# Kernel tuning notes

Measured on AMD Instinct MI355X. Metric: run time of the kernel, lower is better.

The kernel has to match this reference:

```python
import jax, jax.numpy as jnp
import numpy as np

T, B, X, H, Z = 28, 16384, 28, 100, 16
EPS = 1e-10


def setup_inputs() -> dict:
    key = jax.random.key(0)
    ks = jax.random.split(key, 32)
    s = 0.1  # weight scale to keep activations sane
    d = {
        'x': jax.random.uniform(ks[0], (T, B, X), jnp.float32),
        'eps': jax.random.normal(ks[1], (T, B, Z), jnp.float32),
        'Wpx': jax.random.normal(ks[2], (H, X)) * s, 'bpx': jnp.zeros((H,)),
        'Wpz': jax.random.normal(ks[3], (H, Z)) * s, 'bpz': jnp.zeros((H,)),
        'Wp1': jax.random.normal(ks[4], (H, H)) * s, 'bp1': jnp.zeros((H,)),
        'Wp_mu': jax.random.normal(ks[5], (Z, H)) * s, 'bp_mu': jnp.zeros((Z,)),
        'Wp_sig': jax.random.normal(ks[6], (Z, H)) * s, 'bp_sig': jnp.zeros((Z,)),
        'We1': jax.random.normal(ks[7], (H, 2 * H)) * s, 'be1': jnp.zeros((H,)),
        'We_mu': jax.random.normal(ks[8], (Z, H)) * s, 'be_mu': jnp.zeros((Z,)),
        'We_sig': jax.random.normal(ks[9], (Z, H)) * s, 'be_sig': jnp.zeros((Z,)),
        'Wd1': jax.random.normal(ks[10], (H, 2 * H)) * s, 'bd1': jnp.zeros((H,)),
        'Wd2': jax.random.normal(ks[11], (H, H)) * s, 'bd2': jnp.zeros((H,)),
        'Wd3': jax.random.normal(ks[12], (X, H)) * s, 'bd3': jnp.zeros((X,)),
        'Wih': jax.random.normal(ks[13], (3 * H, 2 * H)) * s, 'Whh': jax.random.normal(ks[14], (3 * H, H)) * s,
        'bih': jnp.zeros((3 * H,)), 'bhh': jnp.zeros((3 * H,)),
    }
    return {k: v.astype(jnp.float32) for k, v in d.items()}


def _lin(a, W, b):
    return a @ W.T + b


def reference(x, eps, Wpx, bpx, Wpz, bpz, Wp1, bp1, Wp_mu, bp_mu, Wp_sig, bp_sig,
              We1, be1, We_mu, be_mu, We_sig, be_sig, Wd1, bd1, Wd2, bd2, Wd3, bd3,
              Wih, Whh, bih, bhh):
    def step(h, inp):
        xt, et = inp  # [B,X], [B,Z]
        px = jax.nn.relu(_lin(xt, Wpx, bpx))  # phi_x
        # encoder q(z|x,h)
        he = jax.nn.relu(_lin(jnp.concatenate([px, h], -1), We1, be1))
        enc_mu = _lin(he, We_mu, be_mu)
        enc_sig = jax.nn.softplus(_lin(he, We_sig, be_sig))
        # prior p(z|h)
        hp = jax.nn.relu(_lin(h, Wp1, bp1))
        pr_mu = _lin(hp, Wp_mu, bp_mu)
        pr_sig = jax.nn.softplus(_lin(hp, Wp_sig, bp_sig))
        # reparameterize (torch code uses sqrt(scale) -- treat scale as var)
        z = enc_mu + jnp.sqrt(enc_sig) * et
        pz = jax.nn.relu(_lin(z, Wpz, bpz))  # phi_z
        # decoder p(x|z,h)
        hd = jax.nn.relu(_lin(jnp.concatenate([pz, h], -1), Wd1, bd1))
        hd = jax.nn.relu(_lin(hd, Wd2, bd2))
        probs = jax.nn.sigmoid(_lin(hd, Wd3, bd3))
        # GRUCell(input=[pz, px], h)
        gi = jnp.concatenate([pz, px], -1) @ Wih.T + bih
        gh = h @ Whh.T + bhh
        ir, iu, in_ = jnp.split(gi, 3, -1)
        hr, hu, hn = jnp.split(gh, 3, -1)
        r = jax.nn.sigmoid(ir + hr)
        u = jax.nn.sigmoid(iu + hu)
        n = jnp.tanh(in_ + r * hn)
        h_next = (1.0 - u) * n + u * h
        # KL(enc || prior)
        ps = pr_sig + EPS
        kl = 0.5 * (2 * jnp.log(ps) - 2 * jnp.log(enc_sig)
                    + (enc_sig ** 2 + (enc_mu - pr_mu) ** 2) / ps ** 2 - 1.0)
        kl = kl.sum(1).mean()
        # Bernoulli NLL
        nll = -(xt * jnp.log(probs + EPS) + (1.0 - xt) * jnp.log(1.0 - probs + EPS))
        nll = nll.sum(1).mean()
        return h_next, (kl, nll)

    h0 = jnp.zeros((x.shape[1], H), x.dtype)
    _, (kls, nlls) = jax.lax.scan(step, h0, (x, eps))
    return kls.sum(), nlls.sum()
```

## Files before the change

### kernel.cpp

```cpp
#include <hip/hip_runtime.h>
#include <math.h>

#define DEVFN __device__ __forceinline__

namespace {

typedef __bf16 bf16x8 __attribute__((ext_vector_type(8)));
typedef float  f32x4  __attribute__((ext_vector_type(4)));

constexpr int T = 28, B = 16384, X = 28, H = 100, Z = 16;
constexpr int ROWS = 32;
constexpr int NTH  = 256;
constexpr int ST   = 104;
constexpr int HBUF = ROWS*ST + 24;
constexpr int XST  = 40;
constexpr float KEPS = 1e-10f;

constexpr int FB_PX   = 0;
constexpr int FB_HE   = 7;
constexpr int FB_EMU  = 63;
constexpr int FB_ESIG = 67;
constexpr int FB_HP   = 71;
constexpr int FB_PMU  = 99;
constexpr int FB_PSIG = 103;
constexpr int FB_PZ   = 107;
constexpr int FB_HD1  = 114;
constexpr int FB_HD2  = 170;
constexpr int FB_PRB  = 198;
constexpr int FB_GIR  = 206;
constexpr int FB_GIU  = 262;
constexpr int FB_GIN  = 318;
constexpr int FB_GHR  = 374;
constexpr int FB_GHU  = 402;
constexpr int FB_GHN  = 430;
constexpr int NFRAG   = 458;

struct Params {
  const float *x,*eps,*Wpx,*bpx,*Wpz,*bpz,*Wp1,*bp1,*Wp_mu,*bp_mu,*Wp_sig,*bp_sig,
              *We1,*be1,*We_mu,*be_mu,*We_sig,*be_sig,*Wd1,*bd1,*Wd2,*bd2,*Wd3,*bd3,
              *Wih,*Whh,*bih,*bhh;
  float *out;
};

DEVFN float frcp(float x){ return __builtin_amdgcn_rcpf(x); }
DEVFN float fsigmoid(float v){ return frcp(1.f + __expf(-v)); }
DEVFN float ftanh(float v){
  float t = __expf(-2.f*fabsf(v));
  float r = (1.f - t) * frcp(1.f + t);
  return copysignf(r, v);
}
DEVFN float fsoftplus(float v){
  float sp = (v > 15.f) ? v : __logf(1.f + __expf(v));
  return fmaxf(sp, 1e-6f);
}

DEVFN f32x4 MFMA(bf16x8 a, bf16x8 b, f32x4 c){
  return __builtin_amdgcn_mfma_f32_16x16x32_bf16(a, b, c, 0, 0, 0);
}

__global__ void prep_kernel(Params P, __bf16* FRW)
{
  const int f = blockIdx.x, l = threadIdx.x;
  const int bases[18] = {FB_PX,FB_HE,FB_EMU,FB_ESIG,FB_HP,FB_PMU,FB_PSIG,FB_PZ,FB_HD1,
                         FB_HD2,FB_PRB,FB_GIR,FB_GIU,FB_GIN,FB_GHR,FB_GHU,FB_GHN,NFRAG};
  int li = 0;
  while (f >= bases[li+1]) ++li;

  const float* W; const float* Bv; int KT, N, roff, wstr, vK, mode;
  switch (li) {
    case 0:  W=P.Wpx;    Bv=P.bpx;    KT=1; N=100; roff=0;   wstr=28;  vK=28;  mode=0; break;
    case 1:  W=P.We1;    Bv=P.be1;    KT=8; N=100; roff=0;   wstr=200; vK=100; mode=1; break;
    case 2:  W=P.We_mu;  Bv=P.be_mu;  KT=4; N=16;  roff=0;   wstr=100; vK=100; mode=0; break;
    case 3:  W=P.We_sig; Bv=P.be_sig; KT=4; N=16;  roff=0;   wstr=100; vK=100; mode=0; break;
    case 4:  W=P.Wp1;    Bv=P.bp1;    KT=4; N=100; roff=0;   wstr=100; vK=100; mode=0; break;
    case 5:  W=P.Wp_mu;  Bv=P.bp_mu;  KT=4; N=16;  roff=0;   wstr=100; vK=100; mode=0; break;
    case 6:  W=P.Wp_sig; Bv=P.bp_sig; KT=4; N=16;  roff=0;   wstr=100; vK=100; mode=0; break;
    case 7:  W=P.Wpz;    Bv=P.bpz;    KT=1; N=100; roff=0;   wstr=16;  vK=16;  mode=0; break;
    case 8:  W=P.Wd1;    Bv=P.bd1;    KT=8; N=100; roff=0;   wstr=200; vK=100; mode=1; break;
    case 9:  W=P.Wd2;    Bv=P.bd2;    KT=4; N=100; roff=0;   wstr=100; vK=100; mode=0; break;
    case 10: W=P.Wd3;    Bv=P.bd3;    KT=4; N=28;  roff=0;   wstr=100; vK=100; mode=0; break;
    case 11: W=P.Wih;    Bv=P.bih;    KT=8; N=100; roff=0;   wstr=200; vK=100; mode=1; break;
    case 12: W=P.Wih;    Bv=P.bih;    KT=8; N=100; roff=100; wstr=200; vK=100; mode=1; break;
    case 13: W=P.Wih;    Bv=P.bih;    KT=8; N=100; roff=200; wstr=200; vK=100; mode=1; break;
    case 14: W=P.Whh;    Bv=P.bhh;    KT=4; N=100; roff=0;   wstr=100; vK=100; mode=0; break;
    case 15: W=P.Whh;    Bv=P.bhh;    KT=4; N=100; roff=100; wstr=100; vK=100; mode=0; break;
    default: W=P.Whh;    Bv=P.bhh;    KT=4; N=100; roff=200; wstr=100; vK=100; mode=0; break;
  }
  const int idx = f - bases[li];
  const int nt = idx / KT, kc = idx % KT;
  const int n  = nt*16 + (l & 15);

  bf16x8 v;
  #pragma unroll
  for (int j = 0; j < 8; ++j) {
    int kk  = (mode ? (kc & 3) : kc)*32 + ((l >> 4)*8) + j;
    float w = 0.f;
    if (n < N) {
      if (mode == 0) {
        if (kk < vK)       w = W[(size_t)(roff + n)*wstr + kk];
        else if (kk == vK) w = Bv[roff + n];
      } else {
        int col = (kc < 4 ? 0 : 100) + kk;
        if (kk < 100)                    w = W[(size_t)(roff + n)*wstr + col];
        else if (kc < 4 && kk == 100)    w = Bv[roff + n];
      }
    }
    v[j] = (__bf16)w;
  }
  *((bf16x8*)FRW + (size_t)f*64 + l) = v;
}

template<int NC>
DEVFN void load_afrags2(bf16x8 (&af)[2][NC], const __bf16* A, int stride, int lane)
{
  #pragma unroll
  for (int mh = 0; mh < 2; ++mh) {
    const __bf16* p = A + (size_t)((lane & 15) + mh*16)*stride + ((lane >> 4)*8);
    #pragma unroll
    for (int kc = 0; kc < NC; ++kc) af[mh][kc] = *(const bf16x8*)(p + kc*32);
  }
}

template<int KT>
DEVFN void layerH2(const bf16x8 (&af)[2][KT], const bf16x8* FRbase, __bf16* dst, int sw, int step, int lane)
{
  for (int nt = sw; nt < 7; nt += step) {
    f32x4 ac0 = {0.f,0.f,0.f,0.f}, ac1 = {0.f,0.f,0.f,0.f};
    const bf16x8* wf = FRbase + (size_t)nt*KT*64 + lane;
    #pragma unroll
    for (int kc = 0; kc < KT; ++kc) {
      bf16x8 w = wf[kc*64];
      ac0 = MFMA(af[0][kc], w, ac0);
      ac1 = MFMA(af[1][kc], w, ac1);
    }
    const int col = nt*16 + (lane & 15);
    if (col < H) {
      const int rbase = (lane >> 4)*4;
      #pragma unroll
      for (int r = 0; r < 4; ++r) {
        dst[(size_t)(rbase + r)*ST + col]      = (__bf16)fmaxf(ac0[r], 0.f);
        dst[(size_t)(16 + rbase + r)*ST + col] = (__bf16)fmaxf(ac1[r], 0.f);
      }
    }
  }
}

DEVFN void layerHcat2_1(const bf16x8 (&b0)[2][4], const bf16x8 (&b1)[2][4], const bf16x8* FRbase,
                        __bf16* dst, int nt, int lane)
{
  f32x4 ac0 = {0.f,0.f,0.f,0.f}, ac1 = {0.f,0.f,0.f,0.f};
  const bf16x8* wf = FRbase + (size_t)nt*8*64 + lane;
  #pragma unroll
  for (int kc = 0; kc < 4; ++kc) {
    bf16x8 w = wf[kc*64];
    ac0 = MFMA(b0[0][kc], w, ac0);
    ac1 = MFMA(b0[1][kc], w, ac1);
  }
  #pragma unroll
  for (int kc = 0; kc < 4; ++kc) {
    bf16x8 w = wf[(4+kc)*64];
    ac0 = MFMA(b1[0][kc], w, ac0);
    ac1 = MFMA(b1[1][kc], w, ac1);
  }
  const int col = nt*16 + (lane & 15);
  if (col < H) {
    const int rbase = (lane >> 4)*4;
    #pragma unroll
    for (int r = 0; r < 4; ++r) {
      dst[(size_t)(rbase + r)*ST + col]      = (__bf16)fmaxf(ac0[r], 0.f);
      dst[(size_t)(16 + rbase + r)*ST + col] = (__bf16)fmaxf(ac1[r], 0.f);
    }
  }
}

template<int KT>
DEVFN void head4x2(const bf16x8 (&af)[2][KT], const bf16x8* FRbase, int lane, f32x4& o0, f32x4& o1)
{
  f32x4 ac0 = {0.f,0.f,0.f,0.f}, ac1 = {0.f,0.f,0.f,0.f};
  #pragma unroll
  for (int kc = 0; kc < KT; ++kc) {
    bf16x8 w = FRbase[kc*64 + lane];
    ac0 = MFMA(af[0][kc], w, ac0);
    ac1 = MFMA(af[1][kc], w, ac1);
  }
  o0 = ac0; o1 = ac1;
}

template<int KT>
DEVFN f32x4 head4(const bf16x8 (&af)[KT], const bf16x8* FRbase, int lane)
{
  f32x4 acc = {0.f,0.f,0.f,0.f};
  #pragma unroll
  for (int kc = 0; kc < KT; ++kc) acc = MFMA(af[kc], FRbase[kc*64 + lane], acc);
  return acc;
}

__global__ __launch_bounds__(NTH, 2) void vrnn_kernel(Params P, const __bf16* FRW)
{
  __shared__ alignas(16) __bf16 sPX[HBUF];
  __shared__ alignas(16) __bf16 sPZ[HBUF];
  __shared__ alignas(16) __bf16 sA [HBUF];
  __shared__ alignas(16) __bf16 sB [HBUF];
  __shared__ alignas(16) __bf16 sH0[HBUF];
  __shared__ alignas(16) __bf16 sH1[HBUF];
  __shared__ alignas(16) __bf16 sZ [ROWS*XST];
  __shared__ float sred[8];

  const bf16x8* FR = (const bf16x8*)FRW;
  const int tid  = threadIdx.x;
  const int lane = tid & 63;
  const int wv   = tid >> 6;
  const int gr0  = blockIdx.x * ROWS;

  for (int i = tid; i < HBUF; i += NTH) {
    sPX[i]=(__bf16)0.f; sPZ[i]=(__bf16)0.f; sA[i]=(__bf16)0.f; sB[i]=(__bf16)0.f;
    sH0[i]=(__bf16)0.f; sH1[i]=(__bf16)0.f;
  }
  for (int i = tid; i < ROWS*XST; i += NTH) sZ[i]=(__bf16)0.f;
  __syncthreads();
  if (tid < ROWS) {
    sPX[tid*ST+100]=(__bf16)1.f; sPZ[tid*ST+100]=(__bf16)1.f; sA[tid*ST+100]=(__bf16)1.f;
    sB [tid*ST+100]=(__bf16)1.f; sH0[tid*ST+100]=(__bf16)1.f; sH1[tid*ST+100]=(__bf16)1.f;
    sZ[tid*XST+16]=(__bf16)1.f;
  }
  __syncthreads();

  float kl = 0.f, nll = 0.f;

  for (int t = 0; t < T; ++t) {
    __bf16* sHo = (t & 1) ? sH1 : sH0;
    __bf16* sHn = (t & 1) ? sH0 : sH1;

    {
      bf16x8 ax[2][1];
      #pragma unroll
      for (int mh = 0; mh < 2; ++mh) {
        const float* xr = P.x + ((size_t)t*B + gr0 + mh*16 + (lane & 15))*X + (lane >> 4)*8;
        float4 fa = *(const float4*)xr;
        float4 fb = make_float4(0.f,0.f,0.f,0.f);
        if ((lane >> 4) < 3) fb = *(const float4*)(xr + 4);
        bf16x8 a;
        a[0]=(__bf16)fa.x; a[1]=(__bf16)fa.y; a[2]=(__bf16)fa.z; a[3]=(__bf16)fa.w;
        a[4]=(__bf16)fb.x; a[5]=(__bf16)fb.y; a[6]=(__bf16)fb.z; a[7]=(__bf16)fb.w;
        if ((lane >> 4) == 3) a[4] = (__bf16)1.f;
        ax[mh][0] = a;
      }
      layerH2<1>(ax, FR + (size_t)FB_PX*64, sPX, wv, 4, lane);
      bf16x8 ah[2][4]; load_afrags2(ah, sHo, ST, lane);
      layerH2<4>(ah, FR + (size_t)FB_HP*64, sB, (wv + 1) & 3, 4, lane);
    }
    __syncthreads();

    {
      bf16x8 a0[2][4]; load_afrags2(a0, sPX, ST, lane);
      bf16x8 a1[2][4]; load_afrags2(a1, sHo, ST, lane);
      for (int nt = wv; nt < 7; nt += 4)
        layerHcat2_1(a0, a1, FR + (size_t)FB_HE*64, sA, nt, lane);
    }
    __syncthreads();

    {
      bf16x8 a1[2][4]; load_afrags2(a1, sA, ST, lane);
      bf16x8 a2[2][4]; load_afrags2(a2, sB, ST, lane);
      f32x4 emu[2], esg[2], pmu[2], psg[2];
      head4x2(a1, FR + (size_t)FB_EMU*64,  lane, emu[0], emu[1]);
      head4x2(a1, FR + (size_t)FB_ESIG*64, lane, esg[0], esg[1]);
      head4x2(a2, FR + (size_t)FB_PMU*64,  lane, pmu[0], pmu[1]);
      head4x2(a2, FR + (size_t)FB_PSIG*64, lane, psg[0], psg[1]);
      const int zi = lane & 15;
      const int rbase = (lane >> 4)*4;
      #pragma unroll
      for (int mh = 0; mh < 2; ++mh) {
        #pragma unroll
        for (int r = 0; r < 4; ++r) {
          float em = emu[mh][r];
          float es = fsoftplus(esg[mh][r]);
          float ev = P.eps[((size_t)t*B + gr0 + mh*16 + rbase + r)*Z + zi];
          sZ[(mh*16 + rbase + r)*XST + zi] = (__bf16)(em + __builtin_amdgcn_sqrtf(es)*ev);
          if (r == wv) {
            float ps = fsoftplus(psg[mh][r]) + KEPS;
            float dm = em - pmu[mh][r];
            float rps = frcp(ps);
            kl += 0.5f*(2.f*__logf(ps*frcp(es)) + (es*es + dm*dm)*(rps*rps) - 1.f);
          }
        }
      }
    }

    {
      bf16x8 az[2][1];
      #pragma unroll
      for (int mh = 0; mh < 2; ++mh)
        az[mh][0] = *(const bf16x8*)(sZ + (size_t)((lane & 15) + mh*16)*XST + (lane >> 4)*8);
      layerH2<1>(az, FR + (size_t)FB_PZ*64, sPZ, wv, 4, lane);
    }
    __syncthreads();

    {
      bf16x8 apz[2][4]; load_afrags2(apz, sPZ, ST, lane);
      bf16x8 ah [2][4]; load_afrags2(ah,  sHo, ST, lane);

      if (wv == 3) {
        for (int nt = 0; nt < 7; nt += 2)
          layerHcat2_1(apz, ah, FR + (size_t)FB_HD1*64, sA, nt, lane);
      } else {
        layerHcat2_1(apz, ah, FR + (size_t)FB_HD1*64, sA, 2*wv + 1, lane);
      }

      bf16x8 apx[2][4]; load_afrags2(apx, sPX, ST, lane);

      for (int c = wv; c < 7; c += 4) {
        const f32x4 z4 = {0.f,0.f,0.f,0.f};
        f32x4 gr[2]={z4,z4}, gu[2]={z4,z4}, gn[2]={z4,z4};
        const bf16x8* wr = FR + (size_t)(FB_GIR + c*8)*64 + lane;
        const bf16x8* wu = FR + (size_t)(FB_GIU + c*8)*64 + lane;
        const bf16x8* wn = FR + (size_t)(FB_GIN + c*8)*64 + lane;
        #pragma unroll
        for (int kc = 0; kc < 4; ++kc) {
          bf16x8 wR = wr[kc*64], wU = wu[kc*64], wN = wn[kc*64];
          #pragma unroll
          for (int mh = 0; mh < 2; ++mh) {
            gr[mh] = MFMA(apz[mh][kc], wR, gr[mh]);
            gu[mh] = MFMA(apz[mh][kc], wU, gu[mh]);
            gn[mh] = MFMA(apz[mh][kc], wN, gn[mh]);
          }
        }
        #pragma unroll
        for (int kc = 0; kc < 4; ++kc) {
          bf16x8 wR = wr[(4+kc)*64], wU = wu[(4+kc)*64], wN = wn[(4+kc)*64];
          #pragma unroll
          for (int mh = 0; mh < 2; ++mh) {
            gr[mh] = MFMA(apx[mh][kc], wR, gr[mh]);
            gu[mh] = MFMA(apx[mh][kc], wU, gu[mh]);
            gn[mh] = MFMA(apx[mh][kc], wN, gn[mh]);
          }
        }
        f32x4 hr[2]={z4,z4}, hu[2]={z4,z4}, hn[2]={z4,z4};
        const bf16x8* vr = FR + (size_t)(FB_GHR + c*4)*64 + lane;
        const bf16x8* vu = FR + (size_t)(FB_GHU + c*4)*64 + lane;
        const bf16x8* vn = FR + (size_t)(FB_GHN + c*4)*64 + lane;
        #pragma unroll
        for (int kc = 0; kc < 4; ++kc) {
          bf16x8 wR = vr[kc*64], wU = vu[kc*64], wN = vn[kc*64];
          #pragma unroll
          for (int mh = 0; mh < 2; ++mh) {
            hr[mh] = MFMA(ah[mh][kc], wR, hr[mh]);
            hu[mh] = MFMA(ah[mh][kc], wU, hu[mh]);
            hn[mh] = MFMA(ah[mh][kc], wN, hn[mh]);
          }
        }
        const int n = c*16 + (lane & 15);
        if (n < H) {
          const int rbase = (lane >> 4)*4;
          #pragma unroll
          for (int mh = 0; mh < 2; ++mh) {
            #pragma unroll
            for (int r = 0; r < 4; ++r) {
              float rr = fsigmoid(gr[mh][r] + hr[mh][r]);
              float uu = fsigmoid(gu[mh][r] + hu[mh][r]);
              float nn = ftanh(gn[mh][r] + rr*hn[mh][r]);
              const size_t off = (size_t)(mh*16 + rbase + r)*ST + n;
              float ho = (float)sHo[off];
              sHn[off] = (__bf16)((1.f-uu)*nn + uu*ho);
            }
          }
        }
      }
    }
    __syncthreads();

    {
      bf16x8 af[2][4]; load_afrags2(af, sA, ST, lane);
      layerH2<4>(af, FR + (size_t)FB_HD2*64, sB, wv, 4, lane);
    }
    __syncthreads();

    {
      const int pt = wv & 1;
      const int mh = wv >> 1;
      bf16x8 af[4];
      const __bf16* p = sB + (size_t)((lane & 15) + mh*16)*ST + ((lane >> 4)*8);
      #pragma unroll
      for (int kc = 0; kc < 4; ++kc) af[kc] = *(const bf16x8*)(p + kc*32);
      f32x4 acc = head4(af, FR + (size_t)(FB_PRB + pt*4)*64, lane);
      const int n = pt*16 + (lane & 15);
      if (n < X) {
        const int rbase = (lane >> 4)*4;
        #pragma unroll
        for (int r = 0; r < 4; ++r) {
          float v  = acc[r];
          float xv = P.x[((size_t)t*B + gr0 + mh*16 + rbase + r)*X + n];
          nll += fmaxf(-v, 0.f) + __logf(1.f + __expf(-fabsf(v))) + (1.f - xv)*v;
        }
      }
    }
    __syncthreads();
  }

  for (int off = 32; off > 0; off >>= 1) {
    kl  += __shfl_down(kl,  off);
    nll += __shfl_down(nll, off);
  }
  if (lane == 0) { sred[wv] = kl; sred[4 + wv] = nll; }
  __syncthreads();
  if (tid == 0) {
    atomicAdd(&P.out[0], (sred[0] + sred[1] + sred[2] + sred[3]) * (1.f/(float)B));
    atomicAdd(&P.out[1], (sred[4] + sred[5] + sred[6] + sred[7]) * (1.f/(float)B));
  }
}

}

extern "C" void kernel_launch(void* const* d_in, const int* in_sizes, int n_in,
                              void* d_out, int out_size, void* d_ws, size_t ws_size,
                              hipStream_t stream)
{
  Params p;
  const float* const* f = (const float* const*)d_in;
  p.x=f[0];    p.eps=f[1];
  p.Wpx=f[2];  p.bpx=f[3];   p.Wpz=f[4];   p.bpz=f[5];
  p.Wp1=f[6];  p.bp1=f[7];   p.Wp_mu=f[8]; p.bp_mu=f[9];
  p.Wp_sig=f[10]; p.bp_sig=f[11];
  p.We1=f[12]; p.be1=f[13];  p.We_mu=f[14]; p.be_mu=f[15];
  p.We_sig=f[16]; p.be_sig=f[17];
  p.Wd1=f[18]; p.bd1=f[19];  p.Wd2=f[20];  p.bd2=f[21];
  p.Wd3=f[22]; p.bd3=f[23];
  p.Wih=f[24]; p.Whh=f[25];  p.bih=f[26];  p.bhh=f[27];
  p.out = (float*)d_out;

  hipMemsetAsync(d_out, 0, 2*sizeof(float), stream);
  prep_kernel<<<dim3(NFRAG), dim3(64), 0, stream>>>(p, (__bf16*)d_ws);
  vrnn_kernel<<<dim3(B/ROWS), dim3(NTH), 0, stream>>>(p, (const __bf16*)d_ws);
}
```

Baseline: 671.9 us.

## Hoist GRU hidden-gate MFMAs into earlier phase and double-buffer to drop step-end barrier

The h@Whh gate products are moved out of the GRU phase into the phase that computes phi_z, which lightens the busiest barrier-delimited section and spreads its work across waves. The phi_x and decoder-hidden buffers are double-buffered by timestep parity, so the __syncthreads at the end of each timestep can be removed. In exchange, each wave holds up to 24 more accumulator registers across a barrier and the block uses more LDS, which could hurt occupancy at 2 blocks per CU.

```diff
diff --git a/kernel.cpp b/kernel.cpp
--- a/kernel.cpp
+++ b/kernel.cpp
@@ -195,12 +195,77 @@
   return acc;
 }
 
+DEVFN void gh_tile(int c, const bf16x8 (&ah)[2][4], const bf16x8* FR,
+                   f32x4 (&hr)[2], f32x4 (&hu)[2], f32x4 (&hn)[2], int lane)
+{
+  const bf16x8* vr = FR + (size_t)(FB_GHR + c*4)*64 + lane;
+  const bf16x8* vu = FR + (size_t)(FB_GHU + c*4)*64 + lane;
+  const bf16x8* vn = FR + (size_t)(FB_GHN + c*4)*64 + lane;
+  #pragma unroll
+  for (int kc = 0; kc < 4; ++kc) {
+    bf16x8 wR = vr[kc*64], wU = vu[kc*64], wN = vn[kc*64];
+    #pragma unroll
+    for (int mh = 0; mh < 2; ++mh) {
+      hr[mh] = MFMA(ah[mh][kc], wR, hr[mh]);
+      hu[mh] = MFMA(ah[mh][kc], wU, hu[mh]);
+      hn[mh] = MFMA(ah[mh][kc], wN, hn[mh]);
+    }
+  }
+}
+
+DEVFN void gru_tile(int c, const bf16x8 (&apz)[2][4], const bf16x8 (&apx)[2][4],
+                    const f32x4 (&hr)[2], const f32x4 (&hu)[2], const f32x4 (&hn)[2],
+                    const bf16x8* FR, const __bf16* sHo, __bf16* sHn, int lane)
+{
+  const f32x4 z4 = {0.f,0.f,0.f,0.f};
+  f32x4 gr[2]={z4,z4}, gu[2]={z4,z4}, gn[2]={z4,z4};
+  const bf16x8* wr = FR + (size_t)(FB_GIR + c*8)*64 + lane;
+  const bf16x8* wu = FR + (size_t)(FB_GIU + c*8)*64 + lane;
+  const bf16x8* wn = FR + (size_t)(FB_GIN + c*8)*64 + lane;
+  #pragma unroll
+  for (int kc = 0; kc < 4; ++kc) {
+    bf16x8 wR = wr[kc*64], wU = wu[kc*64], wN = wn[kc*64];
+    #pragma unroll
+    for (int mh = 0; mh < 2; ++mh) {
+      gr[mh] = MFMA(apz[mh][kc], wR, gr[mh]);
+      gu[mh] = MFMA(apz[mh][kc], wU, gu[mh]);
+      gn[mh] = MFMA(apz[mh][kc], wN, gn[mh]);
+    }
+  }
+  #pragma unroll
+  for (int kc = 0; kc < 4; ++kc) {
+    bf16x8 wR = wr[(4+kc)*64], wU = wu[(4+kc)*64], wN = wn[(4+kc)*64];
+    #pragma unroll
+    for (int mh = 0; mh < 2; ++mh) {
+      gr[mh] = MFMA(apx[mh][kc], wR, gr[mh]);
+      gu[mh] = MFMA(apx[mh][kc], wU, gu[mh]);
+      gn[mh] = MFMA(apx[mh][kc], wN, gn[mh]);
+    }
+  }
+  const int n = c*16 + (lane & 15);
+  if (n < H) {
+    const int rbase = (lane >> 4)*4;
+    #pragma unroll
+    for (int mh = 0; mh < 2; ++mh) {
+      #pragma unroll
+      for (int r = 0; r < 4; ++r) {
+        float rr = fsigmoid(gr[mh][r] + hr[mh][r]);
+        float uu = fsigmoid(gu[mh][r] + hu[mh][r]);
+        float nn = ftanh(gn[mh][r] + rr*hn[mh][r]);
+        const size_t off = (size_t)(mh*16 + rbase + r)*ST + n;
+        float ho = (float)sHo[off];
+        sHn[off] = (__bf16)((1.f-uu)*nn + uu*ho);
+      }
+    }
+  }
+}
+
 __global__ __launch_bounds__(NTH, 2) void vrnn_kernel(Params P, const __bf16* FRW)
 {
-  __shared__ alignas(16) __bf16 sPX[HBUF];
+  __shared__ alignas(16) __bf16 sPXb[2][HBUF];
   __shared__ alignas(16) __bf16 sPZ[HBUF];
   __shared__ alignas(16) __bf16 sA [HBUF];
-  __shared__ alignas(16) __bf16 sB [HBUF];
+  __shared__ alignas(16) __bf16 sBb[2][HBUF];
   __shared__ alignas(16) __bf16 sH0[HBUF];
   __shared__ alignas(16) __bf16 sH1[HBUF];
   __shared__ alignas(16) __bf16 sZ [ROWS*XST];
@@ -213,14 +278,16 @@
   const int gr0  = blockIdx.x * ROWS;
 
   for (int i = tid; i < HBUF; i += NTH) {
-    sPX[i]=(__bf16)0.f; sPZ[i]=(__bf16)0.f; sA[i]=(__bf16)0.f; sB[i]=(__bf16)0.f;
-    sH0[i]=(__bf16)0.f; sH1[i]=(__bf16)0.f;
+    sPXb[0][i]=(__bf16)0.f; sPXb[1][i]=(__bf16)0.f; sPZ[i]=(__bf16)0.f; sA[i]=(__bf16)0.f;
+    sBb[0][i]=(__bf16)0.f; sBb[1][i]=(__bf16)0.f; sH0[i]=(__bf16)0.f; sH1[i]=(__bf16)0.f;
   }
   for (int i = tid; i < ROWS*XST; i += NTH) sZ[i]=(__bf16)0.f;
   __syncthreads();
   if (tid < ROWS) {
-    sPX[tid*ST+100]=(__bf16)1.f; sPZ[tid*ST+100]=(__bf16)1.f; sA[tid*ST+100]=(__bf16)1.f;
-    sB [tid*ST+100]=(__bf16)1.f; sH0[tid*ST+100]=(__bf16)1.f; sH1[tid*ST+100]=(__bf16)1.f;
+    sPXb[0][tid*ST+100]=(__bf16)1.f; sPXb[1][tid*ST+100]=(__bf16)1.f;
+    sPZ[tid*ST+100]=(__bf16)1.f; sA[tid*ST+100]=(__bf16)1.f;
+    sBb[0][tid*ST+100]=(__bf16)1.f; sBb[1][tid*ST+100]=(__bf16)1.f;
+    sH0[tid*ST+100]=(__bf16)1.f; sH1[tid*ST+100]=(__bf16)1.f;
     sZ[tid*XST+16]=(__bf16)1.f;
   }
   __syncthreads();
@@ -230,6 +297,8 @@
   for (int t = 0; t < T; ++t) {
     __bf16* sHo = (t & 1) ? sH1 : sH0;
     __bf16* sHn = (t & 1) ? sH0 : sH1;
+    __bf16* sPX = sPXb[t & 1];
+    __bf16* sB  = sBb [t & 1];
 
     {
       bf16x8 ax[2][1];
@@ -287,12 +356,19 @@
       }
     }
 
+    const f32x4 z4 = {0.f,0.f,0.f,0.f};
+    f32x4 hrA[2]={z4,z4}, huA[2]={z4,z4}, hnA[2]={z4,z4};
+    f32x4 hrB[2]={z4,z4}, huB[2]={z4,z4}, hnB[2]={z4,z4};
+
     {
       bf16x8 az[2][1];
       #pragma unroll
       for (int mh = 0; mh < 2; ++mh)
         az[mh][0] = *(const bf16x8*)(sZ + (size_t)((lane & 15) + mh*16)*XST + (lane >> 4)*8);
       layerH2<1>(az, FR + (size_t)FB_PZ*64, sPZ, wv, 4, lane);
+      bf16x8 ah[2][4]; load_afrags2(ah, sHo, ST, lane);
+      gh_tile(wv, ah, FR, hrA, huA, hnA, lane);
+      if (wv < 3) gh_tile(wv + 4, ah, FR, hrB, huB, hnB, lane);
     }
     __syncthreads();
 
@@ -308,64 +384,9 @@
       }
 
       bf16x8 apx[2][4]; load_afrags2(apx, sPX, ST, lane);
-
-      for (int c = wv; c < 7; c += 4) {
-        const f32x4 z4 = {0.f,0.f,0.f,0.f};
-        f32x4 gr[2]={z4,z4}, gu[2]={z4,z4}, gn[2]={z4,z4};
-        const bf16x8* wr = FR + (size_t)(FB_GIR + c*8)*64 + lane;
-        const bf16x8* wu = FR + (size_t)(FB_GIU + c*8)*64 + lane;
-        const bf16x8* wn = FR + (size_t)(FB_GIN + c*8)*64 + lane;
-        #pragma unroll
-        for (int kc = 0; kc < 4; ++kc) {
-          bf16x8 wR = wr[kc*64], wU = wu[kc*64], wN = wn[kc*64];
-          #pragma unroll
-          for (int mh = 0; mh < 2; ++mh) {
-            gr[mh] = MFMA(apz[mh][kc], wR, gr[mh]);
-            gu[mh] = MFMA(apz[mh][kc], wU, gu[mh]);
-            gn[mh] = MFMA(apz[mh][kc], wN, gn[mh]);
-          }
-        }
-        #pragma unroll
-        for (int kc = 0; kc < 4; ++kc) {
-          bf16x8 wR = wr[(4+kc)*64], wU = wu[(4+kc)*64], wN = wn[(4+kc)*64];
-          #pragma unroll
-          for (int mh = 0; mh < 2; ++mh) {
-            gr[mh] = MFMA(apx[mh][kc], wR, gr[mh]);
-            gu[mh] = MFMA(apx[mh][kc], wU, gu[mh]);
-            gn[mh] = MFMA(apx[mh][kc], wN, gn[mh]);
-          }
-        }
-        f32x4 hr[2]={z4,z4}, hu[2]={z4,z4}, hn[2]={z4,z4};
-        const bf16x8* vr = FR + (size_t)(FB_GHR + c*4)*64 + lane;
-        const bf16x8* vu = FR + (size_t)(FB_GHU + c*4)*64 + lane;
-        const bf16x8* vn = FR + (size_t)(FB_GHN + c*4)*64 + lane;
-        #pragma unroll
-        for (int kc = 0; kc < 4; ++kc) {
-          bf16x8 wR = vr[kc*64], wU = vu[kc*64], wN = vn[kc*64];
-          #pragma unroll
-          for (int mh = 0; mh < 2; ++mh) {
-            hr[mh] = MFMA(ah[mh][kc], wR, hr[mh]);
-            hu[mh] = MFMA(ah[mh][kc], wU, hu[mh]);
-            hn[mh] = MFMA(ah[mh][kc], wN, hn[mh]);
-          }
-        }
-        const int n = c*16 + (lane & 15);
-        if (n < H) {
-          const int rbase = (lane >> 4)*4;
-          #pragma unroll
-          for (int mh = 0; mh < 2; ++mh) {
-            #pragma unroll
-            for (int r = 0; r < 4; ++r) {
-              float rr = fsigmoid(gr[mh][r] + hr[mh][r]);
-              float uu = fsigmoid(gu[mh][r] + hu[mh][r]);
-              float nn = ftanh(gn[mh][r] + rr*hn[mh][r]);
-              const size_t off = (size_t)(mh*16 + rbase + r)*ST + n;
-              float ho = (float)sHo[off];
-              sHn[off] = (__bf16)((1.f-uu)*nn + uu*ho);
-            }
-          }
-        }
-      }
+      gru_tile(wv, apz, apx, hrA, huA, hnA, FR, sHo, sHn, lane);
+      if (wv < 3)
+        gru_tile(wv + 4, apz, apx, hrB, huB, hnB, FR, sHo, sHn, lane);
     }
     __syncthreads();
 
@@ -394,8 +415,9 @@
         }
       }
     }
-    __syncthreads();
-  }
+  }
+
+  __syncthreads();
 
   for (int off = 32; off > 0; off >>= 1) {
     kl  += __shfl_down(kl,  off);
```

Measured after the change: 1.071 ms. 59.4% more time.
